# Optimization experiments

Hardware: AMD Instinct MI355X
Metric: run time of the kernel (lower is better)

The kernel has to match this reference:

```python
import jax, jax.numpy as jnp
import numpy as np

STRIDE = 1
PAD = 1
EXTENT = 3  # kernel footprint (ceil of max tap offset), 3x3 tap grid


def setup_inputs() -> dict:
    key = jax.random.key(0)
    k1, k2 = jax.random.split(key)
    B, Cin, H, W = 8, 64, 128, 128
    Cout, K = 64, 9
    x = jax.random.normal(k1, (B, Cin, H, W), dtype=jnp.float32)
    # per-tap weights, one scalar weight per (out_ch, in_ch, tap) -- op formula is 'x * w'
    weights = jax.random.normal(k2, (Cout, Cin, K), dtype=jnp.float32) * 0.05
    # 3x3 integer grid shifted by +0.4 -> non-integer offsets => bilinear (sub-pixel) gather
    base = jnp.stack(jnp.meshgrid(jnp.arange(3.0), jnp.arange(3.0), indexing='ij'), -1).reshape(9, 2)
    tap_offsets = (base + 0.4).astype(jnp.float32)  # [K, 2] (dy, dx)
    return {"x": x, "weights": weights, "tap_offsets": tap_offsets}


def _bilinear_tap(xp, dy, dx, H_out, W_out):
    # Gather xp at (oy*stride + dy, ox*stride + dx) with separable bilinear interp.
    Hp, Wp = xp.shape[-2], xp.shape[-1]
    y = jnp.arange(H_out, dtype=xp.dtype) * STRIDE + dy
    xc = jnp.arange(W_out, dtype=xp.dtype) * STRIDE + dx
    y0 = jnp.floor(y)
    x0 = jnp.floor(xc)
    fy = (y - y0)[None, None, :, None]
    fx = (xc - x0)[None, None, None, :]
    y0i = jnp.clip(y0.astype(jnp.int32), 0, Hp - 1)
    y1i = jnp.clip(y0.astype(jnp.int32) + 1, 0, Hp - 1)
    x0i = jnp.clip(x0.astype(jnp.int32), 0, Wp - 1)
    x1i = jnp.clip(x0.astype(jnp.int32) + 1, 0, Wp - 1)
    # interp rows first: [B, C, H_out, Wp]
    ry = xp[:, :, y0i, :] * (1.0 - fy) + xp[:, :, y1i, :] * fy
    # then columns: [B, C, H_out, W_out]
    return ry[:, :, :, x0i] * (1.0 - fx) + ry[:, :, :, x1i] * fx


def reference(x, weights, tap_offsets):
    B, Cin, H, W = x.shape
    K = weights.shape[-1]
    xp = jnp.pad(x, ((0, 0), (0, 0), (PAD, PAD), (PAD, PAD)))
    H_out = (H + 2 * PAD - EXTENT) // STRIDE + 1
    W_out = (W + 2 * PAD - EXTENT) // STRIDE + 1
    # gather all taps (loop over small fixed K=9, each fully vectorized over B,C,H,W)
    taps = [_bilinear_tap(xp, tap_offsets[k, 0], tap_offsets[k, 1], H_out, W_out)
            for k in range(K)]
    g = jnp.stack(taps, 0)  # [K, B, Cin, H_out, W_out]
    # per-tap op 'x * w', accumulated over taps and input channels
    return jnp.einsum('kbiyx,oik->boyx', g, weights)  # [B, Cout, H_out, W_out]
```

## Files before the change

### kernel.cpp

```cpp
#include <hip/hip_runtime.h>


#define CIN   64
#define COUT  64
#define HH    128
#define WW    128

typedef __attribute__((ext_vector_type(8))) short bf16x8;
typedef __attribute__((ext_vector_type(4))) float f32x4;
typedef __attribute__((ext_vector_type(4))) unsigned int u32x4;

__device__ __forceinline__ unsigned short f2bf(float f) {
  unsigned int u = __float_as_uint(f);
  u = (u + 0x7fffu + ((u >> 16) & 1u)) >> 16;
  return (unsigned short)u;
}

__global__ void make_wb(const float* __restrict__ wgt,
                        const float* __restrict__ off,
                        unsigned short* __restrict__ wb)
{
  int id = blockIdx.x * 64 + threadIdx.x;
  int o = id >> 6, c = id & 63;
  float W16[16];
  #pragma unroll
  for (int i = 0; i < 16; ++i) W16[i] = 0.f;
  for (int k = 0; k < 9; ++k) {
    float dy = off[2*k], dx = off[2*k+1];
    float fyf = floorf(dy), fxf = floorf(dx);
    int   iy = (int)fyf,   ix = (int)fxf;
    float fy = dy - fyf,   fx = dx - fxf;
    float wk = wgt[(o*CIN + c)*9 + k];
    W16[(iy  )*4 + ix  ] += wk * (1.f-fy)*(1.f-fx);
    W16[(iy  )*4 + ix+1] += wk * (1.f-fy)*fx;
    W16[(iy+1)*4 + ix  ] += wk * fy*(1.f-fx);
    W16[(iy+1)*4 + ix+1] += wk * fy*fx;
  }
  for (int rs = 0; rs < 16; ++rs)
    wb[(o*16 + rs)*64 + c] = f2bf(W16[rs]);
}

constexpr int CS    = 40;
constexpr int LCOLS = 132;

__global__ __launch_bounds__(256, 2)
void conv_mfma(const float* __restrict__ x,
               const unsigned short* __restrict__ wb,
               float* __restrict__ out)
{
  __shared__ unsigned short lt[5 * LCOLS * CS];

  const int wg = blockIdx.x;
  const int b  = wg >> 6;
  const int y0 = (wg & 63) * 2;
  const int t  = threadIdx.x;
  const int lane = t & 63;
  const int wave = t >> 6;
  const int m15  = lane & 15;
  const int q    = lane >> 4;

  f32x4 acc[2][2][4];
  #pragma unroll
  for (int xi = 0; xi < 2; ++xi)
    #pragma unroll
    for (int yl = 0; yl < 2; ++yl)
      #pragma unroll
      for (int n = 0; n < 4; ++n)
        acc[xi][yl][n] = (f32x4){0.f, 0.f, 0.f, 0.f};

  #pragma unroll
  for (int p = 0; p < 2; ++p) {
    if (p) __syncthreads();

    if (t < 80) {
      int row  = t >> 4;
      int rem  = t & 15;
      int csel = rem >> 2;
      int col  = (csel == 0) ? 0 : (128 + csel);
      int chnk = rem & 3;
      *(u32x4*)&lt[(row*LCOLS + col)*CS + chnk*8] = (u32x4){0u,0u,0u,0u};
    }

    for (int it = wave; it < 40; it += 4) {
      int row  = it >> 3;
      int rem  = it & 7;
      int chnk = rem >> 1;
      int xh   = rem & 1;
      int xcol = xh*64 + lane;
      int gy   = y0 + row - 1;
      unsigned int pk[4];
      if ((unsigned)gy < (unsigned)HH) {
        const float* ps = x + ((size_t)((b*CIN + p*32 + chnk*8)*HH + gy))*WW + xcol;
        float v[8];
        #pragma unroll
        for (int cc = 0; cc < 8; ++cc) v[cc] = ps[cc*HH*WW];
        #pragma unroll
        for (int i = 0; i < 4; ++i)
          pk[i] = (unsigned int)f2bf(v[2*i]) | ((unsigned int)f2bf(v[2*i+1]) << 16);
      } else {
        pk[0] = pk[1] = pk[2] = pk[3] = 0u;
      }
      *(u32x4*)&lt[(row*LCOLS + xcol + 1)*CS + chnk*8] = *(u32x4*)pk;
    }
    __syncthreads();

    #pragma unroll
    for (int rs = 0; rs < 16; ++rs) {
      const int r = rs >> 2, s = rs & 3;
      bf16x8 bfr[4];
      #pragma unroll
      for (int n = 0; n < 4; ++n)
        bfr[n] = *(const bf16x8*)(wb + ((n*16 + m15)*16 + rs)*64 + p*32 + q*8);
      #pragma unroll
      for (int xi = 0; xi < 2; ++xi) {
        const int xt = wave*2 + xi;
        #pragma unroll
        for (int yl = 0; yl < 2; ++yl) {
          bf16x8 afr = *(const bf16x8*)(&lt[((yl + r)*LCOLS + (xt*16 + m15 + s))*CS + q*8]);
          #pragma unroll
          for (int n = 0; n < 4; ++n)
            acc[xi][yl][n] = __builtin_amdgcn_mfma_f32_16x16x32_bf16(afr, bfr[n], acc[xi][yl][n], 0, 0, 0);
        }
      }
    }
  }

  #pragma unroll
  for (int xi = 0; xi < 2; ++xi) {
    const int xt = wave*2 + xi;
    #pragma unroll
    for (int yl = 0; yl < 2; ++yl) {
      #pragma unroll
      for (int n = 0; n < 4; ++n) {
        int o = n*16 + m15;
        float* dst = out + (((size_t)(b*COUT + o))*HH + (y0 + yl))*WW + xt*16 + q*4;
        *(f32x4*)dst = acc[xi][yl][n];
      }
    }
  }
}

extern "C" void kernel_launch(void* const* d_in, const int* in_sizes, int n_in,
                              void* d_out, int out_size, void* d_ws, size_t ws_size,
                              hipStream_t stream)
{
  const float* x   = (const float*)d_in[0];
  const float* wgt = (const float*)d_in[1];
  const float* off = (const float*)d_in[2];
  float* out = (float*)d_out;
  unsigned short* wb = (unsigned short*)d_ws;

  make_wb<<<64, 64, 0, stream>>>(wgt, off, wb);
  conv_mfma<<<512, 256, 0, stream>>>(x, wb, out);
}
```

Before: 125.5 us.

## Retile conv to one output row per block with swizzled LDS and pre-laid weights

Each block now computes a single output row with 128 threads across 1024 blocks, where before it computed two rows with 256 threads. Block indices are mapped so neighbouring rows land on the same XCD, which should improve L2 reuse of the shared halo rows. The input tile uses an XOR-style slot swizzle in place of padding to avoid LDS bank conflicts. Weights are pre-arranged in MFMA lane order so each lane does one contiguous load. Output is staged through LDS so global stores are coalesced. The cost is that each input row is loaded and converted about four times instead of about two and a half times, which adds redundant global traffic.

Measured after the change: 108.4 us. -13.7%, faster.

```diff
diff --git a/kernel.cpp b/kernel.cpp
--- a/kernel.cpp
+++ b/kernel.cpp
@@ -18,7 +18,7 @@
 
 __global__ void make_wb(const float* __restrict__ wgt,
                         const float* __restrict__ off,
-                        unsigned short* __restrict__ wb)
+                        unsigned short* __restrict__ wb2)
 {
   int id = blockIdx.x * 64 + threadIdx.x;
   int o = id >> 6, c = id & 63;
@@ -36,107 +36,117 @@
     W16[(iy+1)*4 + ix  ] += wk * fy*(1.f-fx);
     W16[(iy+1)*4 + ix+1] += wk * fy*fx;
   }
+  int p = c >> 5, q = (c >> 3) & 3, j = c & 7;
+  int n = o >> 4, m15 = o & 15;
+  int lanei = q*16 + m15;
   for (int rs = 0; rs < 16; ++rs)
-    wb[(o*16 + rs)*64 + c] = f2bf(W16[rs]);
+    wb2[(size_t)(((p*16 + rs)*4 + n)*64 + lanei)*8 + j] = f2bf(W16[rs]);
 }
 
-constexpr int CS    = 40;
-constexpr int LCOLS = 132;
-
-__global__ __launch_bounds__(256, 2)
+__global__ __launch_bounds__(128, 2)
 void conv_mfma(const float* __restrict__ x,
-               const unsigned short* __restrict__ wb,
+               const unsigned short* __restrict__ wb2,
                float* __restrict__ out)
 {
-  __shared__ unsigned short lt[5 * LCOLS * CS];
+  __shared__ unsigned short tile[4 * 132 * 32];
 
-  const int wg = blockIdx.x;
-  const int b  = wg >> 6;
-  const int y0 = (wg & 63) * 2;
-  const int t  = threadIdx.x;
+  const int wg  = blockIdx.x;
+  const int xcd = wg & 7;
+  const int i8  = wg >> 3;
+  const int b   = i8 >> 4;
+  const int y0  = xcd * 16 + (i8 & 15);
+  const int t    = threadIdx.x;
+  const int wave = t >> 6;
   const int lane = t & 63;
-  const int wave = t >> 6;
   const int m15  = lane & 15;
   const int q    = lane >> 4;
 
-  f32x4 acc[2][2][4];
+  f32x4 acc[4][4];
   #pragma unroll
-  for (int xi = 0; xi < 2; ++xi)
+  for (int mi = 0; mi < 4; ++mi)
     #pragma unroll
-    for (int yl = 0; yl < 2; ++yl)
-      #pragma unroll
-      for (int n = 0; n < 4; ++n)
-        acc[xi][yl][n] = (f32x4){0.f, 0.f, 0.f, 0.f};
+    for (int n = 0; n < 4; ++n)
+      acc[mi][n] = (f32x4){0.f, 0.f, 0.f, 0.f};
 
   #pragma unroll
   for (int p = 0; p < 2; ++p) {
     if (p) __syncthreads();
 
-    if (t < 80) {
-      int row  = t >> 4;
-      int rem  = t & 15;
-      int csel = rem >> 2;
+    if (p == 0) {
+      int row = t >> 5, rem = t & 31;
+      int csel = rem >> 3;
       int col  = (csel == 0) ? 0 : (128 + csel);
-      int chnk = rem & 3;
-      *(u32x4*)&lt[(row*LCOLS + col)*CS + chnk*8] = (u32x4){0u,0u,0u,0u};
+      int w8   = rem & 7;
+      *(unsigned long long*)&tile[(row*132 + col)*32 + w8*4] = 0ull;
     }
 
-    for (int it = wave; it < 40; it += 4) {
-      int row  = it >> 3;
-      int rem  = it & 7;
-      int chnk = rem >> 1;
-      int xh   = rem & 1;
-      int xcol = xh*64 + lane;
-      int gy   = y0 + row - 1;
+    #pragma unroll 4
+    for (int it = 0; it < 16; ++it) {
+      int g     = it*2 + wave;
+      int row   = g >> 3;
+      int rem   = g & 7;
+      int chunk = rem >> 1;
+      int xh    = rem & 1;
+      int px    = xh*64 + lane;
+      int gy    = y0 + row - 1;
       unsigned int pk[4];
       if ((unsigned)gy < (unsigned)HH) {
-        const float* ps = x + ((size_t)((b*CIN + p*32 + chnk*8)*HH + gy))*WW + xcol;
+        const float* ps = x + ((size_t)((b*CIN + p*32 + chunk*8)*HH + gy))*WW + px;
         float v[8];
         #pragma unroll
-        for (int cc = 0; cc < 8; ++cc) v[cc] = ps[cc*HH*WW];
+        for (int cc = 0; cc < 8; ++cc) v[cc] = ps[(size_t)cc*HH*WW];
         #pragma unroll
         for (int i = 0; i < 4; ++i)
           pk[i] = (unsigned int)f2bf(v[2*i]) | ((unsigned int)f2bf(v[2*i+1]) << 16);
       } else {
         pk[0] = pk[1] = pk[2] = pk[3] = 0u;
       }
-      *(u32x4*)&lt[(row*LCOLS + xcol + 1)*CS + chnk*8] = *(u32x4*)pk;
+      int pos  = px + 1;
+      int slot = (chunk + (pos >> 2)) & 3;
+      *(u32x4*)&tile[((row*132 + pos)*4 + slot)*8] = *(u32x4*)pk;
     }
     __syncthreads();
 
+    const unsigned short* wstream = wb2 + (size_t)p*16*4*512 + lane*8;
     #pragma unroll
     for (int rs = 0; rs < 16; ++rs) {
       const int r = rs >> 2, s = rs & 3;
       bf16x8 bfr[4];
       #pragma unroll
       for (int n = 0; n < 4; ++n)
-        bfr[n] = *(const bf16x8*)(wb + ((n*16 + m15)*16 + rs)*64 + p*32 + q*8);
+        bfr[n] = *(const bf16x8*)(wstream + (rs*4 + n)*512);
+      bf16x8 afr[4];
       #pragma unroll
-      for (int xi = 0; xi < 2; ++xi) {
-        const int xt = wave*2 + xi;
+      for (int mi = 0; mi < 4; ++mi) {
+        int pos  = wave*64 + mi*16 + m15 + s;
+        int slot = (q + (pos >> 2)) & 3;
+        afr[mi] = *(const bf16x8*)(&tile[((r*132 + pos)*4 + slot)*8]);
+      }
+      #pragma unroll
+      for (int mi = 0; mi < 4; ++mi)
         #pragma unroll
-        for (int yl = 0; yl < 2; ++yl) {
-          bf16x8 afr = *(const bf16x8*)(&lt[((yl + r)*LCOLS + (xt*16 + m15 + s))*CS + q*8]);
-          #pragma unroll
-          for (int n = 0; n < 4; ++n)
-            acc[xi][yl][n] = __builtin_amdgcn_mfma_f32_16x16x32_bf16(afr, bfr[n], acc[xi][yl][n], 0, 0, 0);
-        }
-      }
+        for (int n = 0; n < 4; ++n)
+          acc[mi][n] = __builtin_amdgcn_mfma_f32_16x16x32_bf16(afr[mi], bfr[n], acc[mi][n], 0, 0, 0);
     }
   }
 
+  __syncthreads();
+  float* epi = (float*)tile;
   #pragma unroll
-  for (int xi = 0; xi < 2; ++xi) {
-    const int xt = wave*2 + xi;
+  for (int mi = 0; mi < 4; ++mi)
     #pragma unroll
-    for (int yl = 0; yl < 2; ++yl) {
-      #pragma unroll
-      for (int n = 0; n < 4; ++n) {
-        int o = n*16 + m15;
-        float* dst = out + (((size_t)(b*COUT + o))*HH + (y0 + yl))*WW + xt*16 + q*4;
-        *(f32x4*)dst = acc[xi][yl][n];
-      }
+    for (int n = 0; n < 4; ++n) {
+      int o  = n*16 + m15;
+      int px = wave*64 + mi*16 + q*4;
+      *(f32x4*)&epi[o*132 + px] = acc[mi][n];
     }
+  __syncthreads();
+  #pragma unroll
+  for (int i = 0; i < 16; ++i) {
+    int o  = i*4 + (t >> 5);
+    int px = (t & 31) * 4;
+    f32x4 v = *(const f32x4*)&epi[o*132 + px];
+    *(f32x4*)&out[(((size_t)(b*COUT + o))*HH + y0)*WW + px] = v;
   }
 }
 
@@ -148,8 +158,8 @@
   const float* wgt = (const float*)d_in[1];
   const float* off = (const float*)d_in[2];
   float* out = (float*)d_out;
-  unsigned short* wb = (unsigned short*)d_ws;
+  unsigned short* wb2 = (unsigned short*)d_ws;
 
-  make_wb<<<64, 64, 0, stream>>>(wgt, off, wb);
-  conv_mfma<<<512, 256, 0, stream>>>(x, wb, out);
+  make_wb<<<64, 64, 0, stream>>>(wgt, off, wb2);
+  conv_mfma<<<1024, 128, 0, stream>>>(x, wb2, out);
 }
```

## Retile conv to 4x64 blocks with 32x32x16 MFMA and prepacked weights

Applied to the files above, without the earlier changes.

Each workgroup now covers 4 output rows by 64 columns instead of 2 full rows, and stages all 64 input channels into LDS in a single pass rather than two 32-channel passes. The inner loop switches from 16x16x32 to 32x32x16 bf16 MFMA, and the weights are pre-permuted into lane-major fragments so each lane reads a contiguous 16-byte load. The aim is less redundant halo loading per output, fewer syncs, and more reuse per LDS fragment. In exchange the LDS tile is larger, which may limit occupancy, the boundary loads are now predicated, and the output stores are strided.

Result: faster. 116.8 us (-6.9%).

```diff
diff --git a/kernel.cpp b/kernel.cpp
--- a/kernel.cpp
+++ b/kernel.cpp
@@ -6,9 +6,10 @@
 #define HH    128
 #define WW    128
 
-typedef __attribute__((ext_vector_type(8))) short bf16x8;
-typedef __attribute__((ext_vector_type(4))) float f32x4;
-typedef __attribute__((ext_vector_type(4))) unsigned int u32x4;
+typedef __attribute__((ext_vector_type(8)))  short bf16x8;
+typedef __attribute__((ext_vector_type(4)))  float f32x4;
+typedef __attribute__((ext_vector_type(16))) float f32x16;
+typedef __attribute__((ext_vector_type(4)))  unsigned int u32x4;
 
 __device__ __forceinline__ unsigned short f2bf(float f) {
   unsigned int u = __float_as_uint(f);
@@ -36,105 +37,104 @@
     W16[(iy+1)*4 + ix  ] += wk * fy*(1.f-fx);
     W16[(iy+1)*4 + ix+1] += wk * fy*fx;
   }
-  for (int rs = 0; rs < 16; ++rs)
-    wb[(o*16 + rs)*64 + c] = f2bf(W16[rs]);
+  int g = c >> 4, half = (c >> 3) & 1, j = c & 7;
+  int ni = o >> 5, l31 = o & 31;
+  int lane = half*32 + l31;
+  for (int tap = 0; tap < 16; ++tap) {
+    int h8 = tap >> 3, rs8 = tap & 7;
+    wb[(size_t)((((g*2 + h8)*16) + rs8*2 + ni)*64 + lane)*8 + j] = f2bf(W16[tap]);
+  }
 }
 
-constexpr int CS    = 40;
-constexpr int LCOLS = 132;
+constexpr int CELL = 72;
+constexpr int LPOS = 68;
 
 __global__ __launch_bounds__(256, 2)
 void conv_mfma(const float* __restrict__ x,
                const unsigned short* __restrict__ wb,
                float* __restrict__ out)
 {
-  __shared__ unsigned short lt[5 * LCOLS * CS];
+  __shared__ unsigned short lt[7 * LPOS * CELL];
 
   const int wg = blockIdx.x;
   const int b  = wg >> 6;
-  const int y0 = (wg & 63) * 2;
+  const int y0 = ((wg >> 1) & 31) * 4;
+  const int x0 = (wg & 1) * 64;
   const int t  = threadIdx.x;
+
+  for (int id = t; id < 56 * LPOS; id += 256) {
+    int cg  = id / LPOS;
+    int pos = id - cg * LPOS;
+    int row = cg >> 3;
+    int c8  = cg & 7;
+    int gy  = y0 + row - 1;
+    int gx  = x0 + pos - 1;
+    bool ok = ((unsigned)gy < (unsigned)HH) && ((unsigned)gx < (unsigned)WW);
+    int sgy = ok ? gy : 0, sgx = ok ? gx : 0;
+    float sc = ok ? 1.f : 0.f;
+    const float* ps = x + ((size_t)(b*CIN + c8*8)*HH + sgy)*WW + sgx;
+    float v[8];
+    #pragma unroll
+    for (int cc = 0; cc < 8; ++cc) v[cc] = ps[(size_t)cc*HH*WW] * sc;
+    unsigned int pk[4];
+    #pragma unroll
+    for (int i = 0; i < 4; ++i)
+      pk[i] = (unsigned int)f2bf(v[2*i]) | ((unsigned int)f2bf(v[2*i+1]) << 16);
+    *(u32x4*)&lt[(row*LPOS + pos)*CELL + c8*8] = *(u32x4*)pk;
+  }
+  __syncthreads();
+
   const int lane = t & 63;
   const int wave = t >> 6;
-  const int m15  = lane & 15;
-  const int q    = lane >> 4;
+  const int l31  = lane & 31;
+  const int half = lane >> 5;
 
-  f32x4 acc[2][2][4];
+  f32x16 acc[2][2];
   #pragma unroll
-  for (int xi = 0; xi < 2; ++xi)
+  for (int xh = 0; xh < 2; ++xh)
     #pragma unroll
-    for (int yl = 0; yl < 2; ++yl)
-      #pragma unroll
-      for (int n = 0; n < 4; ++n)
-        acc[xi][yl][n] = (f32x4){0.f, 0.f, 0.f, 0.f};
+    for (int ni = 0; ni < 2; ++ni)
+      acc[xh][ni] = (f32x16)(0.f);
+
+  const unsigned short* wl = wb + lane*8;
 
   #pragma unroll
-  for (int p = 0; p < 2; ++p) {
-    if (p) __syncthreads();
-
-    if (t < 80) {
-      int row  = t >> 4;
-      int rem  = t & 15;
-      int csel = rem >> 2;
-      int col  = (csel == 0) ? 0 : (128 + csel);
-      int chnk = rem & 3;
-      *(u32x4*)&lt[(row*LCOLS + col)*CS + chnk*8] = (u32x4){0u,0u,0u,0u};
-    }
-
-    for (int it = wave; it < 40; it += 4) {
-      int row  = it >> 3;
-      int rem  = it & 7;
-      int chnk = rem >> 1;
-      int xh   = rem & 1;
-      int xcol = xh*64 + lane;
-      int gy   = y0 + row - 1;
-      unsigned int pk[4];
-      if ((unsigned)gy < (unsigned)HH) {
-        const float* ps = x + ((size_t)((b*CIN + p*32 + chnk*8)*HH + gy))*WW + xcol;
-        float v[8];
+  for (int g = 0; g < 4; ++g) {
+    #pragma unroll
+    for (int h8 = 0; h8 < 2; ++h8) {
+      bf16x8 bfr[8][2];
+      #pragma unroll
+      for (int rs8 = 0; rs8 < 8; ++rs8)
         #pragma unroll
-        for (int cc = 0; cc < 8; ++cc) v[cc] = ps[cc*HH*WW];
+        for (int ni = 0; ni < 2; ++ni)
+          bfr[rs8][ni] = *(const bf16x8*)(wl + (size_t)(((g*2 + h8)*16) + rs8*2 + ni)*512);
+      #pragma unroll
+      for (int rs8 = 0; rs8 < 8; ++rs8) {
+        const int tap = h8*8 + rs8;
+        const int r = tap >> 2, sx = tap & 3;
         #pragma unroll
-        for (int i = 0; i < 4; ++i)
-          pk[i] = (unsigned int)f2bf(v[2*i]) | ((unsigned int)f2bf(v[2*i+1]) << 16);
-      } else {
-        pk[0] = pk[1] = pk[2] = pk[3] = 0u;
-      }
-      *(u32x4*)&lt[(row*LCOLS + xcol + 1)*CS + chnk*8] = *(u32x4*)pk;
-    }
-    __syncthreads();
-
-    #pragma unroll
-    for (int rs = 0; rs < 16; ++rs) {
-      const int r = rs >> 2, s = rs & 3;
-      bf16x8 bfr[4];
-      #pragma unroll
-      for (int n = 0; n < 4; ++n)
-        bfr[n] = *(const bf16x8*)(wb + ((n*16 + m15)*16 + rs)*64 + p*32 + q*8);
-      #pragma unroll
-      for (int xi = 0; xi < 2; ++xi) {
-        const int xt = wave*2 + xi;
-        #pragma unroll
-        for (int yl = 0; yl < 2; ++yl) {
-          bf16x8 afr = *(const bf16x8*)(&lt[((yl + r)*LCOLS + (xt*16 + m15 + s))*CS + q*8]);
-          #pragma unroll
-          for (int n = 0; n < 4; ++n)
-            acc[xi][yl][n] = __builtin_amdgcn_mfma_f32_16x16x32_bf16(afr, bfr[n], acc[xi][yl][n], 0, 0, 0);
+        for (int xh = 0; xh < 2; ++xh) {
+          bf16x8 afr = *(const bf16x8*)
+            &lt[((wave + r)*LPOS + (xh*32 + l31 + sx))*CELL + g*16 + half*8];
+          acc[xh][0] = __builtin_amdgcn_mfma_f32_32x32x16_bf16(afr, bfr[rs8][0], acc[xh][0], 0, 0, 0);
+          acc[xh][1] = __builtin_amdgcn_mfma_f32_32x32x16_bf16(afr, bfr[rs8][1], acc[xh][1], 0, 0, 0);
         }
       }
     }
   }
 
+  const int y = y0 + wave;
   #pragma unroll
-  for (int xi = 0; xi < 2; ++xi) {
-    const int xt = wave*2 + xi;
+  for (int xh = 0; xh < 2; ++xh) {
     #pragma unroll
-    for (int yl = 0; yl < 2; ++yl) {
+    for (int ni = 0; ni < 2; ++ni) {
+      int o = ni*32 + l31;
+      float* dst = out + (((size_t)(b*COUT + o))*HH + y)*WW + x0 + xh*32 + 4*half;
       #pragma unroll
-      for (int n = 0; n < 4; ++n) {
-        int o = n*16 + m15;
-        float* dst = out + (((size_t)(b*COUT + o))*HH + (y0 + yl))*WW + xt*16 + q*4;
-        *(f32x4*)dst = acc[xi][yl][n];
+      for (int rg = 0; rg < 4; ++rg) {
+        f32x4 v = (f32x4){acc[xh][ni][4*rg+0], acc[xh][ni][4*rg+1],
+                          acc[xh][ni][4*rg+2], acc[xh][ni][4*rg+3]};
+        *(f32x4*)(dst + 8*rg) = v;
       }
     }
   }
```
